# Optimization experiments

Hardware: AMD Instinct MI355X
Metric: run time of the kernel (lower is better)

Reference implementation:

```python
import jax, jax.numpy as jnp
import numpy as np
import math

HIDDEN = 2048
HEADS = 16
GROUPS = 4
HEAD_DIM = HIDDEN // HEADS  # 128
KV_DIM = GROUPS * HEAD_DIM  # 512
B, S = 2, 2048


def setup_inputs() -> dict:
    key = jax.random.key(0)
    ks = jax.random.split(key, 10)
    scale = 0.02
    return {
        "X": jax.random.normal(ks[0], (B, S, HIDDEN), dtype=jnp.float32),
        "attention_mask": jnp.ones((B, S), dtype=jnp.int32),
        "Wq": jax.random.normal(ks[1], (HIDDEN, HIDDEN), dtype=jnp.float32) * scale,
        "bq": jnp.zeros((HIDDEN,), dtype=jnp.float32),
        "Wk": jax.random.normal(ks[2], (HIDDEN, KV_DIM), dtype=jnp.float32) * scale,
        "bk": jnp.zeros((KV_DIM,), dtype=jnp.float32),
        "Wv": jax.random.normal(ks[3], (HIDDEN, KV_DIM), dtype=jnp.float32) * scale,
        "bv": jnp.zeros((KV_DIM,), dtype=jnp.float32),
        "Wo": jax.random.normal(ks[4], (HIDDEN, HIDDEN), dtype=jnp.float32) * scale,
        "bo": jnp.zeros((HIDDEN,), dtype=jnp.float32),
    }


def reference(X, attention_mask, Wq, bq, Wk, bk, Wv, bv, Wo, bo):
    b, s, _ = X.shape
    num_per_group = HEADS // GROUPS
    # projections
    Q = (X @ Wq + bq).reshape(b, s, HEADS, HEAD_DIM).transpose(0, 2, 1, 3)   # [b,H,s,d]
    K = (X @ Wk + bk).reshape(b, s, GROUPS, HEAD_DIM).transpose(0, 2, 1, 3)  # [b,G,s,d]
    V = (X @ Wv + bv).reshape(b, s, GROUPS, HEAD_DIM).transpose(0, 2, 1, 3)
    # torch .repeat(1, num_per_group, 1, 1) tiles group axis: [g0..gG-1, g0..gG-1, ...]
    K = jnp.tile(K, (1, num_per_group, 1, 1))  # [b,H,s,d]
    V = jnp.tile(V, (1, num_per_group, 1, 1))
    scores = jnp.einsum("bhqd,bhkd->bhqk", Q, K) / math.sqrt(HEAD_DIM)
    mask = attention_mask[:, None, None, :] == 0  # [b,1,1,s]
    scores = jnp.where(mask, jnp.float32(-jnp.inf), scores)
    attn = jax.nn.softmax(scores, axis=-1)
    out = jnp.einsum("bhqk,bhkd->bhqd", attn, V)  # [b,H,s,d]
    out = out.transpose(0, 2, 1, 3).reshape(b, s, HIDDEN)
    return out @ Wo + bo
```

## Files before the change

kernel.cpp:

```cpp
#include <hip/hip_runtime.h>
#include <hip/hip_bf16.h>


typedef __attribute__((ext_vector_type(8))) short short8;
typedef __attribute__((ext_vector_type(4))) short short4v;
typedef __attribute__((ext_vector_type(4))) float float4v;
typedef __attribute__((ext_vector_type(16))) float float16v;

#define C1F 0.12751743f
#define B0F -16.0f

#if defined(__has_builtin) && __has_builtin(__builtin_amdgcn_exp2f)
#define EXP2(x) __builtin_amdgcn_exp2f(x)
#else
#define EXP2(x) exp2f(x)
#endif

__device__ __forceinline__ short f2bf(float x) {
    __hip_bfloat16 h = __float2bfloat16(x);
    short s; __builtin_memcpy(&s, &h, sizeof(s)); return s;
}

__device__ __forceinline__ void gl16(const short* g, short* l) {
    __builtin_amdgcn_global_load_lds(
        (const __attribute__((address_space(1))) void*)g,
        (__attribute__((address_space(3))) void*)l, 16, 0, 0);
}

__global__ __launch_bounds__(256) void prep_kernel(
    const float* __restrict__ X, short* __restrict__ Xb,
    const float* __restrict__ Wq, const float* __restrict__ Wk,
    const float* __restrict__ Wv, const float* __restrict__ Wo,
    short* __restrict__ WqkvT, short* __restrict__ Wot) {
    __shared__ float tile[32][33];
    const int bxg = blockIdx.x;
    if (bxg < 8192) {
        int i = (bxg * 256 + threadIdx.x) * 4;
        float4 v = *(const float4*)(X + i);
        short4v o;
        o[0] = f2bf(v.x); o[1] = f2bf(v.y); o[2] = f2bf(v.z); o[3] = f2bf(v.w);
        *(short4v*)(Xb + i) = o;
        return;
    }
    const int tid = bxg - 8192;
    int bx = tid % 160;
    const int k0 = (tid / 160) * 32;
    const float* W; short* Wt; int N;
    if (bx < 64)      { W = Wq; Wt = WqkvT;                      N = 2048; }
    else if (bx < 80) { W = Wk; Wt = WqkvT + (size_t)2048 * 2048; N = 512; bx -= 64; }
    else if (bx < 96) { W = Wv; Wt = WqkvT + (size_t)2560 * 2048; N = 512; bx -= 80; }
    else              { W = Wo; Wt = Wot;                        N = 2048; bx -= 96; }
    const int K = 2048;
    const int n0 = bx * 32;
    const int tx = threadIdx.x & 31, ty = threadIdx.x >> 5;
#pragma unroll
    for (int i = 0; i < 4; ++i) {
        int kk = ty + i * 8;
        tile[kk][tx] = W[(size_t)(k0 + kk) * N + n0 + tx];
    }
    __syncthreads();
#pragma unroll
    for (int i = 0; i < 4; ++i) {
        int nn = ty + i * 8;
        Wt[(size_t)(n0 + nn) * K + k0 + tx] = f2bf(tile[tx][nn]);
    }
}

__global__ __launch_bounds__(256) void gemm_dma_kernel(
    const short* __restrict__ A, const short* __restrict__ Bt,
    const float* __restrict__ b0, const float* __restrict__ b1, const float* __restrict__ b2,
    short* __restrict__ O0, short* __restrict__ O1, short* __restrict__ O2,
    float* __restrict__ Of, int K, int mode) {
    __shared__ short As[128 * 64];
    __shared__ short Bs[128 * 64];
    const int t = threadIdx.x, lane = t & 63, w = t >> 6;
    const int l15 = lane & 15, quad = lane >> 4;
    const int wm = (w & 1) * 64, wn = (w >> 1) * 64;

    const int nwg = gridDim.x * gridDim.y;
    int bid = blockIdx.y * gridDim.x + blockIdx.x;
    bid = (bid & 7) * (nwg >> 3) + (bid >> 3);
    const int m0 = (bid / gridDim.x) * 128, n0 = (bid % gridDim.x) * 128;

    const int r8 = lane >> 3;
    const int csw = ((lane & 7) ^ r8) * 8;
    const short* ga = A + (size_t)(m0 + w * 8 + r8) * K + csw;
    const short* gb = Bt + (size_t)(n0 + w * 8 + r8) * K + csw;
    short* lA = As + (w * 8) * 64;
    short* lB = Bs + (w * 8) * 64;
    const int xs = l15 & 7;

    float4v acc[4][4] = {};

    for (int k0 = 0; k0 < K; k0 += 64) {
#pragma unroll
        for (int c = 0; c < 4; ++c) {
            gl16(ga + k0 + (size_t)(c * 32) * K, lA + c * 2048);
            gl16(gb + k0 + (size_t)(c * 32) * K, lB + c * 2048);
        }
        __syncthreads();
#pragma unroll
        for (int ks = 0; ks < 2; ++ks) {
            short8 af[4], bfr[4];
            const int ps = ((ks * 4 + quad) ^ xs) * 8;
#pragma unroll
            for (int i = 0; i < 4; ++i)
                af[i] = *(const short8*)(As + (wm + i * 16 + l15) * 64 + ps);
#pragma unroll
            for (int j = 0; j < 4; ++j)
                bfr[j] = *(const short8*)(Bs + (wn + j * 16 + l15) * 64 + ps);
#pragma unroll
            for (int i = 0; i < 4; ++i)
#pragma unroll
                for (int j = 0; j < 4; ++j)
                    acc[i][j] = __builtin_amdgcn_mfma_f32_16x16x32_bf16(af[i], bfr[j], acc[i][j], 0, 0, 0);
        }
        __syncthreads();
    }

#pragma unroll
    for (int i = 0; i < 4; ++i) {
#pragma unroll
        for (int j = 0; j < 4; ++j) {
            const int col = n0 + wn + j * 16 + l15;
            const int row0 = m0 + wm + i * 16 + quad * 4;
            if (mode == 1) {
                const float bc = b0[col];
#pragma unroll
                for (int r = 0; r < 4; ++r)
                    Of[(size_t)(row0 + r) * 2048 + col] = acc[i][j][r] + bc;
            } else if (col < 2048) {
                const float bc = b0[col];
#pragma unroll
                for (int r = 0; r < 4; ++r)
                    O0[(size_t)(row0 + r) * 2048 + col] = f2bf(acc[i][j][r] + bc);
            } else if (col < 2560) {
                const int c = col - 2048;
                const float bc = b1[c];
#pragma unroll
                for (int r = 0; r < 4; ++r)
                    O1[(size_t)(row0 + r) * 512 + c] = f2bf(acc[i][j][r] + bc);
            } else {
                const int c = col - 2560;
                const float bc = b2[c];
                const int qsw = ((quad & 1) << 1) | (quad >> 1);
                const int prow = m0 + wm + i * 16 + qsw * 4;
                short4v ov;
#pragma unroll
                for (int r = 0; r < 4; ++r) ov[r] = f2bf(acc[i][j][r] + bc);
                *(short4v*)(O2 + (size_t)c * 4096 + prow) = ov;
            }
        }
    }
}

__global__ __launch_bounds__(256, 2) void flash_kernel(
    const short* __restrict__ Qb, const short* __restrict__ Kb,
    const short* __restrict__ Vt, const int* __restrict__ mask,
    short* __restrict__ Ab) {
    __shared__ short Ks[2][64 * 136];
    __shared__ short Vs[2][128 * 72];

    const int t = threadIdx.x;
    const int lane = t & 63, w = t >> 6;
    const int l31 = lane & 31, hi = lane >> 5;
    const int qt = blockIdx.x, g = blockIdx.y, b = blockIdx.z;
    const int h = g + 4 * w;
    const int q0 = qt * 32;

    short8 qf[8];
#pragma unroll
    for (int dd = 0; dd < 8; ++dd)
        qf[dd] = *(const short8*)(Qb + (size_t)(b * 2048 + q0 + l31) * 2048
                                  + h * 128 + dd * 16 + hi * 8);

    float16v o[4] = {};
    float rsum = 0.f;

    const int kR = t >> 4, kC = (t & 15) * 8;
    const int vR = t >> 3, vC = (t & 7) * 8;
    const short* kg = Kb + (size_t)(b * 2048 + kR) * 512 + g * 128 + kC;
    const short* vg = Vt + (size_t)(g * 128 + vR) * 4096 + (size_t)b * 2048 + vC;

    short8 kv[4], vv[4];
    int mvr = 1;

#define LOADT(KB)                                                                  \
    do {                                                                           \
        kv[0] = *(const short8*)(kg + (size_t)(KB) * 512);                         \
        kv[1] = *(const short8*)(kg + (size_t)((KB) + 16) * 512);                  \
        kv[2] = *(const short8*)(kg + (size_t)((KB) + 32) * 512);                  \
        kv[3] = *(const short8*)(kg + (size_t)((KB) + 48) * 512);                  \
        vv[0] = *(const short8*)(vg + (KB));                                       \
        vv[1] = *(const short8*)(vg + (size_t)32 * 4096 + (KB));                   \
        vv[2] = *(const short8*)(vg + (size_t)64 * 4096 + (KB));                   \
        vv[3] = *(const short8*)(vg + (size_t)96 * 4096 + (KB));                   \
        mvr = mask[b * 2048 + (KB) + lane];                                        \
    } while (0)

#define STAGE(BUF)                                                                 \
    do {                                                                           \
        _Pragma("unroll")                                                          \
        for (int i_ = 0; i_ < 4; ++i_)                                             \
            *(short8*)(&Ks[BUF][(kR + i_ * 16) * 136 + kC]) = kv[i_];              \
        _Pragma("unroll")                                                          \
        for (int i_ = 0; i_ < 4; ++i_)                                             \
            *(short8*)(&Vs[BUF][(vR + i_ * 32) * 72 + vC]) = vv[i_];               \
    } while (0)

    LOADT(0);
    STAGE(0);
    unsigned long long bits = __ballot(mvr != 0);
    LOADT(64);
    __syncthreads();

    int cur = 0;
    unsigned long long bits_next = bits;

    for (int kt = 0; kt < 32; ++kt) {
        if (kt + 1 < 32) {
            STAGE(cur ^ 1);
            bits_next = __ballot(mvr != 0);
            if (kt + 2 < 32) LOADT((kt + 2) * 64);
        }
        const short* Ksb = &Ks[cur][0];
        const short* Vsb = &Vs[cur][0];

        float16v st0 = {}, st1 = {};
        __builtin_amdgcn_s_setprio(1);
#pragma unroll
        for (int dd = 0; dd < 8; ++dd) {
            short8 kf0 = *(const short8*)(Ksb + l31 * 136 + dd * 16 + hi * 8);
            short8 kf1 = *(const short8*)(Ksb + (32 + l31) * 136 + dd * 16 + hi * 8);
            st0 = __builtin_amdgcn_mfma_f32_32x32x16_bf16(kf0, qf[dd], st0, 0, 0, 0);
            st1 = __builtin_amdgcn_mfma_f32_32x32x16_bf16(kf1, qf[dd], st1, 0, 0, 0);
        }
        __builtin_amdgcn_s_setprio(0);

        const bool full = (bits == ~0ull);
        const unsigned int mlo = ((unsigned int)bits) >> (4 * hi);
        const unsigned int mhi = ((unsigned int)(bits >> 32)) >> (4 * hi);

        if (full) {
#pragma unroll
            for (int e = 0; e < 16; ++e) {
                float p0 = EXP2(fmaf(st0[e], C1F, B0F));
                rsum += p0; st0[e] = p0;
            }
        } else {
#pragma unroll
            for (int e = 0; e < 16; ++e) {
                const int koff = (e & 3) + 8 * (e >> 2);
                float p0 = EXP2(fmaf(st0[e], C1F, B0F));
                p0 = ((mlo >> koff) & 1) ? p0 : 0.f;
                rsum += p0; st0[e] = p0;
            }
        }

        __builtin_amdgcn_s_setprio(1);
#pragma unroll
        for (int cc = 0; cc < 2; ++cc) {
            short8 pa;
#pragma unroll
            for (int e = 0; e < 8; ++e) pa[e] = f2bf(st0[cc * 8 + e]);
#pragma unroll
            for (int db = 0; db < 4; ++db) {
                short8 vb = *(const short8*)(Vsb + (db * 32 + l31) * 72 + cc * 16 + hi * 8);
                o[db] = __builtin_amdgcn_mfma_f32_32x32x16_bf16(pa, vb, o[db], 0, 0, 0);
            }
        }
        __builtin_amdgcn_s_setprio(0);

        if (full) {
#pragma unroll
            for (int e = 0; e < 16; ++e) {
                float p1 = EXP2(fmaf(st1[e], C1F, B0F));
                rsum += p1; st1[e] = p1;
            }
        } else {
#pragma unroll
            for (int e = 0; e < 16; ++e) {
                const int koff = (e & 3) + 8 * (e >> 2);
                float p1 = EXP2(fmaf(st1[e], C1F, B0F));
                p1 = ((mhi >> koff) & 1) ? p1 : 0.f;
                rsum += p1; st1[e] = p1;
            }
        }

        __builtin_amdgcn_s_setprio(1);
#pragma unroll
        for (int cc = 2; cc < 4; ++cc) {
            short8 pa;
#pragma unroll
            for (int e = 0; e < 8; ++e) pa[e] = f2bf(st1[(cc & 1) * 8 + e]);
#pragma unroll
            for (int db = 0; db < 4; ++db) {
                short8 vb = *(const short8*)(Vsb + (db * 32 + l31) * 72 + cc * 16 + hi * 8);
                o[db] = __builtin_amdgcn_mfma_f32_32x32x16_bf16(pa, vb, o[db], 0, 0, 0);
            }
        }
        __builtin_amdgcn_s_setprio(0);

        __syncthreads();
        bits = bits_next;
        cur ^= 1;
    }
#undef LOADT
#undef STAGE

    rsum += __shfl_xor(rsum, 32, 64);
    const float rinv = (rsum > 0.f) ? 1.f / rsum : 0.f;
    float rq[16];
#pragma unroll
    for (int e = 0; e < 16; ++e) {
        const int koff = (e & 3) + 8 * (e >> 2);
        rq[e] = __shfl(rinv, koff + 4 * hi, 64);
    }
    const size_t ob = (size_t)(b * 2048 + q0) * 2048 + h * 128;
#pragma unroll
    for (int db = 0; db < 4; ++db)
#pragma unroll
        for (int e = 0; e < 16; ++e) {
            const int koff = (e & 3) + 8 * (e >> 2);
            Ab[ob + (size_t)(koff + 4 * hi) * 2048 + db * 32 + l31] =
                f2bf(o[db][e] * rq[e]);
        }
}

extern "C" void kernel_launch(void* const* d_in, const int* in_sizes, int n_in,
                              void* d_out, int out_size, void* d_ws, size_t ws_size,
                              hipStream_t stream) {
    (void)in_sizes; (void)n_in; (void)out_size; (void)ws_size;
    const float* X  = (const float*)d_in[0];
    const int* mask = (const int*)d_in[1];
    const float* Wq = (const float*)d_in[2];
    const float* bq = (const float*)d_in[3];
    const float* Wk = (const float*)d_in[4];
    const float* bk = (const float*)d_in[5];
    const float* Wv = (const float*)d_in[6];
    const float* bv = (const float*)d_in[7];
    const float* Wo = (const float*)d_in[8];
    const float* bo = (const float*)d_in[9];
    float* out = (float*)d_out;

    char* ws = (char*)d_ws;
    short* Xb     = (short*)(ws + 0);
    short* WqkvT  = (short*)(ws + 16777216);
    short* Wot    = (short*)(ws + 29360128);
    short* Qb     = (short*)(ws + 37748736);
    short* Kb     = (short*)(ws + 54525952);
    short* Vt     = (short*)(ws + 58720256);
    short* Ab     = Xb;

    const int HID = 2048;

    prep_kernel<<<18432, 256, 0, stream>>>(X, Xb, Wq, Wk, Wv, Wo, WqkvT, Wot);

    gemm_dma_kernel<<<dim3(24, 32), 256, 0, stream>>>(
        Xb, WqkvT, bq, bk, bv, Qb, Kb, Vt, nullptr, HID, 0);

    flash_kernel<<<dim3(64, 4, 2), 256, 0, stream>>>(Qb, Kb, Vt, mask, Ab);

    gemm_dma_kernel<<<dim3(16, 32), 256, 0, stream>>>(
        Ab, Wot, bo, nullptr, nullptr, nullptr, nullptr, nullptr, out, HID, 1);
}
```

Before: 304.7 us.

## Store K/V in MFMA-fragment order and read them directly, dropping LDS staging

The QKV projection epilogue now writes K and V in a pre-swizzled layout that matches the MFMA operand fragments, so each lane's 16-byte load is contiguous. The flash kernel drops the shared-memory double buffer and per-tile __syncthreads and loads K and V fragments straight from global memory into registers. Blocks are remapped with group and batch in the low bits so neighbouring blocks share the same K/V tiles in L2. This removes LDS traffic and barriers, but each of the four waves now fetches the K/V tile itself, global-load latency is exposed without explicit prefetch, and holding 16 V fragments raises register pressure.

```diff
diff --git a/kernel.cpp b/kernel.cpp
--- a/kernel.cpp
+++ b/kernel.cpp
@@ -136,35 +136,42 @@
                     O0[(size_t)(row0 + r) * 2048 + col] = f2bf(acc[i][j][r] + bc);
             } else if (col < 2560) {
                 const int c = col - 2048;
+                const int gk = c >> 7, d = c & 127;
+                const int d16 = d >> 3, dj = d & 7;
                 const float bc = b1[c];
 #pragma unroll
-                for (int r = 0; r < 4; ++r)
-                    O1[(size_t)(row0 + r) * 512 + c] = f2bf(acc[i][j][r] + bc);
+                for (int r = 0; r < 4; ++r) {
+                    const int tok = row0 + r;
+                    const int bb = tok >> 11, key = tok & 2047;
+                    O1[((size_t)((gk * 2 + bb) * 16 + d16) * 2048 + key) * 8 + dj] =
+                        f2bf(acc[i][j][r] + bc);
+                }
             } else {
                 const int c = col - 2560;
+                const int gv = c >> 7, d = c & 127;
                 const float bc = b2[c];
                 const int qsw = ((quad & 1) << 1) | (quad >> 1);
-                const int prow = m0 + wm + i * 16 + qsw * 4;
+                const int slot0 = m0 + wm + i * 16 + qsw * 4;
+                const int bb = slot0 >> 11, s = slot0 & 2047;
+                const int sg = s >> 3, sj0 = s & 7;
                 short4v ov;
 #pragma unroll
                 for (int r = 0; r < 4; ++r) ov[r] = f2bf(acc[i][j][r] + bc);
-                *(short4v*)(O2 + (size_t)c * 4096 + prow) = ov;
+                *(short4v*)(O2 + ((size_t)((gv * 2 + bb) * 256 + sg) * 128 + d) * 8 + sj0) = ov;
             }
         }
     }
 }
 
 __global__ __launch_bounds__(256, 2) void flash_kernel(
-    const short* __restrict__ Qb, const short* __restrict__ Kb,
-    const short* __restrict__ Vt, const int* __restrict__ mask,
+    const short* __restrict__ Qb, const short* __restrict__ Kf,
+    const short* __restrict__ Vf, const int* __restrict__ mask,
     short* __restrict__ Ab) {
-    __shared__ short Ks[2][64 * 136];
-    __shared__ short Vs[2][128 * 72];
-
     const int t = threadIdx.x;
     const int lane = t & 63, w = t >> 6;
     const int l31 = lane & 31, hi = lane >> 5;
-    const int qt = blockIdx.x, g = blockIdx.y, b = blockIdx.z;
+    const int bid = blockIdx.x;
+    const int g = bid & 3, b = (bid >> 2) & 1, qt = bid >> 3;
     const int h = g + 4 * w;
     const int q0 = qt * 32;
 
@@ -177,66 +184,33 @@
     float16v o[4] = {};
     float rsum = 0.f;
 
-    const int kR = t >> 4, kC = (t & 15) * 8;
-    const int vR = t >> 3, vC = (t & 7) * 8;
-    const short* kg = Kb + (size_t)(b * 2048 + kR) * 512 + g * 128 + kC;
-    const short* vg = Vt + (size_t)(g * 128 + vR) * 4096 + (size_t)b * 2048 + vC;
-
-    short8 kv[4], vv[4];
-    int mvr = 1;
-
-#define LOADT(KB)                                                                  \
-    do {                                                                           \
-        kv[0] = *(const short8*)(kg + (size_t)(KB) * 512);                         \
-        kv[1] = *(const short8*)(kg + (size_t)((KB) + 16) * 512);                  \
-        kv[2] = *(const short8*)(kg + (size_t)((KB) + 32) * 512);                  \
-        kv[3] = *(const short8*)(kg + (size_t)((KB) + 48) * 512);                  \
-        vv[0] = *(const short8*)(vg + (KB));                                       \
-        vv[1] = *(const short8*)(vg + (size_t)32 * 4096 + (KB));                   \
-        vv[2] = *(const short8*)(vg + (size_t)64 * 4096 + (KB));                   \
-        vv[3] = *(const short8*)(vg + (size_t)96 * 4096 + (KB));                   \
-        mvr = mask[b * 2048 + (KB) + lane];                                        \
-    } while (0)
-
-#define STAGE(BUF)                                                                 \
-    do {                                                                           \
-        _Pragma("unroll")                                                          \
-        for (int i_ = 0; i_ < 4; ++i_)                                             \
-            *(short8*)(&Ks[BUF][(kR + i_ * 16) * 136 + kC]) = kv[i_];              \
-        _Pragma("unroll")                                                          \
-        for (int i_ = 0; i_ < 4; ++i_)                                             \
-            *(short8*)(&Vs[BUF][(vR + i_ * 32) * 72 + vC]) = vv[i_];               \
-    } while (0)
-
-    LOADT(0);
-    STAGE(0);
-    unsigned long long bits = __ballot(mvr != 0);
-    LOADT(64);
-    __syncthreads();
-
-    int cur = 0;
-    unsigned long long bits_next = bits;
+    const short* kfl = Kf + (size_t)(g * 2 + b) * 16 * 2048 * 8 + hi * 16384 + l31 * 8;
+    const short* vfl = Vf + (size_t)(g * 2 + b) * 256 * 1024 + hi * 1024 + l31 * 8;
+    const int* mp = mask + b * 2048 + lane;
 
     for (int kt = 0; kt < 32; ++kt) {
-        if (kt + 1 < 32) {
-            STAGE(cur ^ 1);
-            bits_next = __ballot(mvr != 0);
-            if (kt + 2 < 32) LOADT((kt + 2) * 64);
-        }
-        const short* Ksb = &Ks[cur][0];
-        const short* Vsb = &Vs[cur][0];
+        const int kb = kt * 64;
+        const int mvr = mp[kb];
+
+        short8 vr[16];
+#pragma unroll
+        for (int cc = 0; cc < 4; ++cc)
+#pragma unroll
+            for (int db = 0; db < 4; ++db)
+                vr[cc * 4 + db] = *(const short8*)(vfl + kb * 128 + cc * 2048 + db * 256);
 
         float16v st0 = {}, st1 = {};
         __builtin_amdgcn_s_setprio(1);
 #pragma unroll
         for (int dd = 0; dd < 8; ++dd) {
-            short8 kf0 = *(const short8*)(Ksb + l31 * 136 + dd * 16 + hi * 8);
-            short8 kf1 = *(const short8*)(Ksb + (32 + l31) * 136 + dd * 16 + hi * 8);
+            short8 kf0 = *(const short8*)(kfl + dd * 32768 + kb * 8);
+            short8 kf1 = *(const short8*)(kfl + dd * 32768 + kb * 8 + 256);
             st0 = __builtin_amdgcn_mfma_f32_32x32x16_bf16(kf0, qf[dd], st0, 0, 0, 0);
             st1 = __builtin_amdgcn_mfma_f32_32x32x16_bf16(kf1, qf[dd], st1, 0, 0, 0);
         }
         __builtin_amdgcn_s_setprio(0);
 
+        const unsigned long long bits = __ballot(mvr != 0);
         const bool full = (bits == ~0ull);
         const unsigned int mlo = ((unsigned int)bits) >> (4 * hi);
         const unsigned int mhi = ((unsigned int)(bits >> 32)) >> (4 * hi);
@@ -264,10 +238,8 @@
 #pragma unroll
             for (int e = 0; e < 8; ++e) pa[e] = f2bf(st0[cc * 8 + e]);
 #pragma unroll
-            for (int db = 0; db < 4; ++db) {
-                short8 vb = *(const short8*)(Vsb + (db * 32 + l31) * 72 + cc * 16 + hi * 8);
-                o[db] = __builtin_amdgcn_mfma_f32_32x32x16_bf16(pa, vb, o[db], 0, 0, 0);
-            }
+            for (int db = 0; db < 4; ++db)
+                o[db] = __builtin_amdgcn_mfma_f32_32x32x16_bf16(pa, vr[cc * 4 + db], o[db], 0, 0, 0);
         }
         __builtin_amdgcn_s_setprio(0);
 
@@ -294,19 +266,11 @@
 #pragma unroll
             for (int e = 0; e < 8; ++e) pa[e] = f2bf(st1[(cc & 1) * 8 + e]);
 #pragma unroll
-            for (int db = 0; db < 4; ++db) {
-                short8 vb = *(const short8*)(Vsb + (db * 32 + l31) * 72 + cc * 16 + hi * 8);
-                o[db] = __builtin_amdgcn_mfma_f32_32x32x16_bf16(pa, vb, o[db], 0, 0, 0);
-            }
+            for (int db = 0; db < 4; ++db)
+                o[db] = __builtin_amdgcn_mfma_f32_32x32x16_bf16(pa, vr[cc * 4 + db], o[db], 0, 0, 0);
         }
         __builtin_amdgcn_s_setprio(0);
-
-        __syncthreads();
-        bits = bits_next;
-        cur ^= 1;
-    }
-#undef LOADT
-#undef STAGE
+    }
 
     rsum += __shfl_xor(rsum, 32, 64);
     const float rinv = (rsum > 0.f) ? 1.f / rsum : 0.f;
@@ -348,8 +312,8 @@
     short* WqkvT  = (short*)(ws + 16777216);
     short* Wot    = (short*)(ws + 29360128);
     short* Qb     = (short*)(ws + 37748736);
-    short* Kb     = (short*)(ws + 54525952);
-    short* Vt     = (short*)(ws + 58720256);
+    short* Kf     = (short*)(ws + 54525952);
+    short* Vf     = (short*)(ws + 58720256);
     short* Ab     = Xb;
 
     const int HID = 2048;
@@ -357,9 +321,9 @@
     prep_kernel<<<18432, 256, 0, stream>>>(X, Xb, Wq, Wk, Wv, Wo, WqkvT, Wot);
 
     gemm_dma_kernel<<<dim3(24, 32), 256, 0, stream>>>(
-        Xb, WqkvT, bq, bk, bv, Qb, Kb, Vt, nullptr, HID, 0);
-
-    flash_kernel<<<dim3(64, 4, 2), 256, 0, stream>>>(Qb, Kb, Vt, mask, Ab);
+        Xb, WqkvT, bq, bk, bv, Qb, Kf, Vf, nullptr, HID, 0);
+
+    flash_kernel<<<512, 256, 0, stream>>>(Qb, Kf, Vf, mask, Ab);
 
     gemm_dma_kernel<<<dim3(16, 32), 256, 0, stream>>>(
         Ab, Wot, bo, nullptr, nullptr, nullptr, nullptr, nullptr, out, HID, 1);
```

New measurement: 342.0 us. +12.2%, slower.

## Stage K/V tiles via direct global-to-LDS loads with XOR-swizzled layout

Applied to the files above, without the earlier changes.

Replaces the register-staged K/V prefetch (global load into registers, then LDS store) in the flash attention kernel with global_load_lds direct-to-LDS transfers. The padded LDS rows are dropped in favour of an XOR swizzle of 16-byte chunks to avoid bank conflicts. The mask ballot now happens at use time. This frees registers and removes LDS store instructions, but prefetch depth drops from two tiles ahead to one and relies on the barrier to cover DMA latency.

```diff
diff --git a/kernel.cpp b/kernel.cpp
--- a/kernel.cpp
+++ b/kernel.cpp
@@ -158,8 +158,8 @@
     const short* __restrict__ Qb, const short* __restrict__ Kb,
     const short* __restrict__ Vt, const int* __restrict__ mask,
     short* __restrict__ Ab) {
-    __shared__ short Ks[2][64 * 136];
-    __shared__ short Vs[2][128 * 72];
+    __shared__ short Ks[2][64 * 128];
+    __shared__ short Vs[2][128 * 64];
 
     const int t = threadIdx.x;
     const int lane = t & 63, w = t >> 6;
@@ -177,51 +177,38 @@
     float16v o[4] = {};
     float rsum = 0.f;
 
-    const int kR = t >> 4, kC = (t & 15) * 8;
-    const int vR = t >> 3, vC = (t & 7) * 8;
-    const short* kg = Kb + (size_t)(b * 2048 + kR) * 512 + g * 128 + kC;
-    const short* vg = Vt + (size_t)(g * 128 + vR) * 4096 + (size_t)b * 2048 + vC;
-
-    short8 kv[4], vv[4];
-    int mvr = 1;
-
-#define LOADT(KB)                                                                  \
+    const int krow = w * 4 + (lane >> 4);
+    const int kgc = (lane & 15) ^ (krow & 7);
+    const short* kgsrc = Kb + (size_t)(b * 2048 + krow) * 512 + g * 128 + kgc * 8;
+    const int vrow = w * 8 + (lane >> 3);
+    const int vgc = (lane & 7) ^ (vrow & 7);
+    const short* vgsrc = Vt + (size_t)(g * 128 + vrow) * 4096 + b * 2048 + vgc * 8;
+    const int* mp = mask + b * 2048 + lane;
+    const int xk = l31 & 7;
+
+#define STAGE_DMA(BUF, KB)                                                         \
     do {                                                                           \
-        kv[0] = *(const short8*)(kg + (size_t)(KB) * 512);                         \
-        kv[1] = *(const short8*)(kg + (size_t)((KB) + 16) * 512);                  \
-        kv[2] = *(const short8*)(kg + (size_t)((KB) + 32) * 512);                  \
-        kv[3] = *(const short8*)(kg + (size_t)((KB) + 48) * 512);                  \
-        vv[0] = *(const short8*)(vg + (KB));                                       \
-        vv[1] = *(const short8*)(vg + (size_t)32 * 4096 + (KB));                   \
-        vv[2] = *(const short8*)(vg + (size_t)64 * 4096 + (KB));                   \
-        vv[3] = *(const short8*)(vg + (size_t)96 * 4096 + (KB));                   \
-        mvr = mask[b * 2048 + (KB) + lane];                                        \
-    } while (0)
-
-#define STAGE(BUF)                                                                 \
-    do {                                                                           \
+        short* KsB = &Ks[BUF][w * 512];                                            \
+        short* VsB = &Vs[BUF][w * 512];                                            \
         _Pragma("unroll")                                                          \
         for (int i_ = 0; i_ < 4; ++i_)                                             \
-            *(short8*)(&Ks[BUF][(kR + i_ * 16) * 136 + kC]) = kv[i_];              \
+            gl16(kgsrc + (size_t)((KB) + i_ * 16) * 512, KsB + i_ * 2048);         \
         _Pragma("unroll")                                                          \
         for (int i_ = 0; i_ < 4; ++i_)                                             \
-            *(short8*)(&Vs[BUF][(vR + i_ * 32) * 72 + vC]) = vv[i_];               \
+            gl16(vgsrc + (KB) + (size_t)(i_ * 32) * 4096, VsB + i_ * 2048);        \
     } while (0)
 
-    LOADT(0);
-    STAGE(0);
-    unsigned long long bits = __ballot(mvr != 0);
-    LOADT(64);
+    STAGE_DMA(0, 0);
+    int mvr = mp[0];
     __syncthreads();
 
     int cur = 0;
-    unsigned long long bits_next = bits;
 
     for (int kt = 0; kt < 32; ++kt) {
+        int mvr_next = 0;
         if (kt + 1 < 32) {
-            STAGE(cur ^ 1);
-            bits_next = __ballot(mvr != 0);
-            if (kt + 2 < 32) LOADT((kt + 2) * 64);
+            STAGE_DMA(cur ^ 1, (kt + 1) * 64);
+            mvr_next = mp[(kt + 1) * 64];
         }
         const short* Ksb = &Ks[cur][0];
         const short* Vsb = &Vs[cur][0];
@@ -230,13 +217,15 @@
         __builtin_amdgcn_s_setprio(1);
 #pragma unroll
         for (int dd = 0; dd < 8; ++dd) {
-            short8 kf0 = *(const short8*)(Ksb + l31 * 136 + dd * 16 + hi * 8);
-            short8 kf1 = *(const short8*)(Ksb + (32 + l31) * 136 + dd * 16 + hi * 8);
+            const int c0 = ((dd * 2 + hi) ^ xk) * 8;
+            short8 kf0 = *(const short8*)(Ksb + l31 * 128 + c0);
+            short8 kf1 = *(const short8*)(Ksb + (32 + l31) * 128 + c0);
             st0 = __builtin_amdgcn_mfma_f32_32x32x16_bf16(kf0, qf[dd], st0, 0, 0, 0);
             st1 = __builtin_amdgcn_mfma_f32_32x32x16_bf16(kf1, qf[dd], st1, 0, 0, 0);
         }
         __builtin_amdgcn_s_setprio(0);
 
+        const unsigned long long bits = __ballot(mvr != 0);
         const bool full = (bits == ~0ull);
         const unsigned int mlo = ((unsigned int)bits) >> (4 * hi);
         const unsigned int mhi = ((unsigned int)(bits >> 32)) >> (4 * hi);
@@ -265,7 +254,8 @@
             for (int e = 0; e < 8; ++e) pa[e] = f2bf(st0[cc * 8 + e]);
 #pragma unroll
             for (int db = 0; db < 4; ++db) {
-                short8 vb = *(const short8*)(Vsb + (db * 32 + l31) * 72 + cc * 16 + hi * 8);
+                const int vc = ((cc * 2 + hi) ^ xk) * 8;
+                short8 vb = *(const short8*)(Vsb + (db * 32 + l31) * 64 + vc);
                 o[db] = __builtin_amdgcn_mfma_f32_32x32x16_bf16(pa, vb, o[db], 0, 0, 0);
             }
         }
@@ -295,18 +285,18 @@
             for (int e = 0; e < 8; ++e) pa[e] = f2bf(st1[(cc & 1) * 8 + e]);
 #pragma unroll
             for (int db = 0; db < 4; ++db) {
-                short8 vb = *(const short8*)(Vsb + (db * 32 + l31) * 72 + cc * 16 + hi * 8);
+                const int vc = ((cc * 2 + hi) ^ xk) * 8;
+                short8 vb = *(const short8*)(Vsb + (db * 32 + l31) * 64 + vc);
                 o[db] = __builtin_amdgcn_mfma_f32_32x32x16_bf16(pa, vb, o[db], 0, 0, 0);
             }
         }
         __builtin_amdgcn_s_setprio(0);
 
         __syncthreads();
-        bits = bits_next;
+        mvr = mvr_next;
         cur ^= 1;
     }
-#undef LOADT
-#undef STAGE
+#undef STAGE_DMA
 
     rsum += __shfl_xor(rsum, 32, 64);
     const float rinv = (rsum > 0.f) ? 1.f / rsum : 0.f;
```

After: 314.7 us. 3.3% more time.
